# Optimization experiments

Hardware: AMD Instinct MI355X
Metric: run time of the kernel (lower is better)

The kernel has to match this reference:

```python
import jax, jax.numpy as jnp
import numpy as np

D_MODEL = 1024
N_HEADS = 16
D_K = D_MODEL // N_HEADS
EPS = 1e-8


def _l2_rownorm(x):
    # RowNormActivation: normalize each row (last dim) to unit L2 norm
    return x * jax.lax.rsqrt(jnp.sum(x * x, axis=-1, keepdims=True) + EPS)


def setup_inputs() -> dict:
    key = jax.random.key(0)
    ks = jax.random.split(key, 11)
    B, S = 2, 2048
    sc = 1.0 / np.sqrt(D_MODEL)
    inp = {
        "Q": jax.random.normal(ks[0], (B, S, D_MODEL), jnp.float32),
        "K": jax.random.normal(ks[1], (B, S, D_MODEL), jnp.float32),
        "V": jax.random.normal(ks[2], (B, S, D_MODEL), jnp.float32),
        "Wq_w": jax.random.normal(ks[3], (D_MODEL, D_MODEL), jnp.float32) * sc,
        "Wq_b": jnp.zeros((D_MODEL,), jnp.float32),
        "Wk_w": jax.random.normal(ks[4], (D_MODEL, D_MODEL), jnp.float32) * sc,
        "Wk_b": jnp.zeros((D_MODEL,), jnp.float32),
        "Wv_w": jax.random.normal(ks[5], (D_MODEL, D_MODEL), jnp.float32) * sc,
        "Wv_b": jnp.zeros((D_MODEL,), jnp.float32),
        "Wo_w": jax.random.normal(ks[6], (D_MODEL, D_MODEL), jnp.float32) * sc,
        "Wo_b": jnp.zeros((D_MODEL,), jnp.float32),
    }
    return inp


def reference(Q, K, V, Wq_w, Wq_b, Wk_w, Wk_b, Wv_w, Wv_b, Wo_w, Wo_b):
    B, S, _ = Q.shape
    # torch Linear: y = x @ W.T + b
    q = (Q @ Wq_w.T + Wq_b).reshape(B, S, N_HEADS, D_K).transpose(0, 2, 1, 3)
    k = (K @ Wk_w.T + Wk_b).reshape(B, S, N_HEADS, D_K).transpose(0, 2, 1, 3)
    v = (V @ Wv_w.T + Wv_b).reshape(B, S, N_HEADS, D_K).transpose(0, 2, 1, 3)
    qn = _l2_rownorm(q)
    kn = _l2_rownorm(k)
    scores = jnp.einsum("bhqd,bhkd->bhqk", qn, kn)
    attn = scores * scores  # squared similarity, no softmax (dropout=0 / eval)
    out = jnp.einsum("bhqk,bhkd->bhqd", attn, v)
    out = out.transpose(0, 2, 1, 3).reshape(B, S, D_MODEL)
    return out @ Wo_w.T + Wo_b
```

## Files before the change

kernel.cpp:

```cpp
#include <hip/hip_runtime.h>
#include <hip/hip_bf16.h>


#define D_MODEL 1024
#define N_HEADS 16
#define D_K     64
#define BATCH   2
#define SEQ     2048
#define M_TOT   (BATCH * SEQ)

typedef short  s16x8 __attribute__((ext_vector_type(8)));
typedef float  f32x4 __attribute__((ext_vector_type(4)));
typedef unsigned short ushort_t;
typedef ushort_t us4 __attribute__((ext_vector_type(4)));

__device__ __forceinline__ ushort_t f2bf(float f) {
    union { float f; unsigned int u; } x; x.f = f;
    unsigned int u = x.u;
    return (ushort_t)((u + 0x7fffu + ((u >> 16) & 1u)) >> 16);
}
__device__ __forceinline__ float bf2f(ushort_t h) {
    union { unsigned int u; float f; } x; x.u = ((unsigned int)h) << 16;
    return x.f;
}
__device__ __forceinline__ unsigned int pack2bf(float a, float b) {
    union { __hip_bfloat162 h; unsigned int u; } x;
    x.h = __float22bfloat162_rn(float2{a, b});
    return x.u;
}

__device__ __forceinline__ void gload_lds16(const ushort_t* g, ushort_t* l) {
    __builtin_amdgcn_global_load_lds(
        (__attribute__((address_space(1))) void*)(ushort_t*)g,
        (__attribute__((address_space(3))) void*)l, 16, 0, 0);
}

#define WAIT_VM(n)  asm volatile("s_waitcnt vmcnt(" #n ")" ::: "memory")
#define WAIT_LGKM0  asm volatile("s_waitcnt lgkmcnt(0)" ::: "memory")
#define BARRIER     asm volatile("s_barrier" ::: "memory")

struct ConvArgs {
    const float* src[11];
    ushort_t*    dst[11];
    int          n[11];
};

__global__ __launch_bounds__(256) void convert_kernel(ConvArgs a) {
    const int t = blockIdx.y;
    const int i = (blockIdx.x * 256 + threadIdx.x) * 4;
    if (i >= a.n[t]) return;
    const float4 v = *(const float4*)(a.src[t] + i);
    us4 p;
    p[0] = f2bf(v.x); p[1] = f2bf(v.y); p[2] = f2bf(v.z); p[3] = f2bf(v.w);
    *(us4*)(a.dst[t] + i) = p;
}

template <int BM, int MODE>
__device__ __forceinline__ void gemm_body(
    ushort_t* __restrict__ smem,
    const ushort_t* __restrict__ A,
    const ushort_t* __restrict__ W,
    const ushort_t* __restrict__ bias,
    ushort_t* __restrict__ out,
    float* __restrict__ outf,
    int bx, int by)
{
    static_assert(BM == 64 || BM == 128, "");
    constexpr int K    = 1024;
    constexpr int MF   = BM / 32;
    constexpr int BUFW = (BM + 128) * 64;
    constexpr int NIT  = K / 64;

    const int t    = threadIdx.x;
    const int wave = t >> 6;
    const int lane = t & 63;
    const int quad = lane >> 4;
    const int lc   = lane & 15;
    const int wm   = wave >> 1;
    const int wn   = wave & 1;
    const int m0   = bx * BM;
    const int n0   = by * 128;

    f32x4 acc[MF][4];
    const f32x4 zero = {0.f, 0.f, 0.f, 0.f};
#pragma unroll
    for (int i = 0; i < MF; ++i)
#pragma unroll
        for (int j = 0; j < 4; ++j) acc[i][j] = zero;

    auto stage = [&](int buf, int k0) {
        ushort_t* Ast = smem + buf * BUFW;
        ushort_t* Bst = Ast + BM * 64;
#pragma unroll
        for (int c = 0; c < MF; ++c) {
            int idx = c * 256 + t;
            int row = idx >> 3, phys = idx & 7;
            int col = (phys ^ (row & 7)) * 8;
            gload_lds16(A + (size_t)(m0 + row) * K + k0 + col, Ast + idx * 8);
        }
#pragma unroll
        for (int c = 0; c < 4; ++c) {
            int idx = c * 256 + t;
            int row = idx >> 3, phys = idx & 7;
            int col = (phys ^ (row & 7)) * 8;
            gload_lds16(W + (size_t)(n0 + row) * K + k0 + col, Bst + idx * 8);
        }
    };
    auto comp = [&](int buf) {
        ushort_t* Ast = smem + buf * BUFW;
        ushort_t* Bst = Ast + BM * 64;
#pragma unroll
        for (int ks = 0; ks < 2; ++ks) {
            const int ph = ((ks * 4 + quad) ^ (lc & 7)) * 8;
            s16x8 a[MF], b[4];
#pragma unroll
            for (int i = 0; i < MF; ++i)
                a[i] = *(const s16x8*)(Ast + (wm * (BM / 2) + i * 16 + lc) * 64 + ph);
#pragma unroll
            for (int i = 0; i < 4; ++i)
                b[i] = *(const s16x8*)(Bst + (wn * 64 + i * 16 + lc) * 64 + ph);
#pragma unroll
            for (int mf = 0; mf < MF; ++mf)
#pragma unroll
                for (int nf = 0; nf < 4; ++nf)
                    acc[mf][nf] = __builtin_amdgcn_mfma_f32_16x16x32_bf16(
                        a[mf], b[nf], acc[mf][nf], 0, 0, 0);
        }
    };

    stage(0, 0);
    stage(1, 64);
    for (int it = 0; it < NIT - 2; ++it) {
        if constexpr (BM == 128) WAIT_VM(8); else WAIT_VM(6);
        BARRIER;
        comp(it & 1);
        WAIT_LGKM0;
        BARRIER;
        stage(it & 1, (it + 2) * 64);
    }
    if constexpr (BM == 128) WAIT_VM(8); else WAIT_VM(6);
    BARRIER;
    comp((NIT - 2) & 1);
    WAIT_VM(0);
    BARRIER;
    comp((NIT - 1) & 1);

    float bv[4];
#pragma unroll
    for (int nf = 0; nf < 4; ++nf) bv[nf] = bf2f(bias[n0 + wn * 64 + nf * 16 + lc]);

    if (MODE == 0) {
#pragma unroll
        for (int mf = 0; mf < MF; ++mf)
#pragma unroll
            for (int nf = 0; nf < 4; ++nf)
#pragma unroll
                for (int r = 0; r < 4; ++r) {
                    int mg = m0 + wm * (BM / 2) + mf * 16 + quad * 4 + r;
                    int ng = n0 + wn * 64 + nf * 16 + lc;
                    outf[(size_t)mg * D_MODEL + ng] = acc[mf][nf][r] + bv[nf];
                }
    } else if (MODE == 1) {
#pragma unroll
        for (int mf = 0; mf < MF; ++mf)
#pragma unroll
            for (int r = 0; r < 4; ++r) {
                float ss = 0.f;
#pragma unroll
                for (int nf = 0; nf < 4; ++nf) {
                    float v = acc[mf][nf][r] + bv[nf];
                    acc[mf][nf][r] = v;
                    ss += v * v;
                }
                ss += __shfl_xor(ss, 1);
                ss += __shfl_xor(ss, 2);
                ss += __shfl_xor(ss, 4);
                ss += __shfl_xor(ss, 8);
                float inv = rsqrtf(ss + 1e-8f);
                int mg = m0 + wm * (BM / 2) + mf * 16 + quad * 4 + r;
                int b  = mg >> 11;
                int s  = mg & 2047;
#pragma unroll
                for (int nf = 0; nf < 4; ++nf) {
                    int ng = n0 + wn * 64 + nf * 16 + lc;
                    int h = ng >> 6, d = ng & 63;
                    out[(((size_t)(b * N_HEADS + h)) * SEQ + s) * D_K + d] =
                        f2bf(acc[mf][nf][r] * inv);
                }
            }
    } else {
        __syncthreads();
        ushort_t* vt = smem + wave * (64 * 72);
#pragma unroll
        for (int mf = 0; mf < 4; ++mf)
#pragma unroll
            for (int nf = 0; nf < 4; ++nf) {
                us4 p;
#pragma unroll
                for (int r = 0; r < 4; ++r) p[r] = f2bf(acc[mf][nf][r] + bv[nf]);
                *(us4*)(vt + (nf * 16 + lc) * 72 + mf * 16 + quad * 4) = p;
            }
        WAIT_LGKM0;
#pragma unroll
        for (int r = 0; r < 8; ++r) {
            int d  = r * 8 + (lane >> 3);
            int so = (lane & 7) * 8;
            uint4 val = *(const uint4*)(vt + d * 72 + so);
            int mg = m0 + wm * 64 + so;
            int b  = mg >> 11;
            int s  = mg & 2047;
            int ng = n0 + wn * 64 + d;
            int h = ng >> 6, dh = ng & 63;
            *(uint4*)(out + (((size_t)(b * N_HEADS + h)) * D_K + dh) * SEQ + s) = val;
        }
    }
}

__global__ __launch_bounds__(256) void qkv_kernel(
    const ushort_t* __restrict__ Qb, const ushort_t* __restrict__ Kb,
    const ushort_t* __restrict__ Vb,
    const ushort_t* __restrict__ Wq, const ushort_t* __restrict__ Wk,
    const ushort_t* __restrict__ Wv,
    const ushort_t* __restrict__ bq, const ushort_t* __restrict__ bk,
    const ushort_t* __restrict__ bv,
    ushort_t* __restrict__ qn, ushort_t* __restrict__ kn,
    ushort_t* __restrict__ vT)
{
    __shared__ __align__(16) ushort_t smem[2 * (128 + 128) * 64];
    const int z = blockIdx.z;
    if (z == 0)
        gemm_body<128, 1>(smem, Qb, Wq, bq, qn, nullptr, blockIdx.x, blockIdx.y);
    else if (z == 1)
        gemm_body<128, 1>(smem, Kb, Wk, bk, kn, nullptr, blockIdx.x, blockIdx.y);
    else
        gemm_body<128, 2>(smem, Vb, Wv, bv, vT, nullptr, blockIdx.x, blockIdx.y);
}

__global__ __launch_bounds__(256) void wo_kernel(
    const ushort_t* __restrict__ A, const ushort_t* __restrict__ W,
    const ushort_t* __restrict__ bias, float* __restrict__ outf)
{
    __shared__ __align__(16) ushort_t smem[2 * (64 + 128) * 64];
    gemm_body<64, 0>(smem, A, W, bias, nullptr, outf, blockIdx.x, blockIdx.y);
}

__global__ __launch_bounds__(256) void attn_kernel(
    const ushort_t* __restrict__ qn,
    const ushort_t* __restrict__ kn,
    const ushort_t* __restrict__ vT,
    ushort_t* __restrict__ attn_out)
{
    __shared__ __align__(16) ushort_t smem[2 * 8192];
    __shared__ __align__(16) ushort_t Pl[128 * 64];

    const int t    = threadIdx.x;
    const int wave = t >> 6;
    const int lane = t & 63;
    const int quad = lane >> 4;
    const int lc   = lane & 15;
    const int bh   = blockIdx.x;
    const int qt   = blockIdx.y;
    const int b    = bh >> 4;
    const int h    = bh & 15;

    const ushort_t* qb = qn + (size_t)bh * SEQ * D_K;
    const ushort_t* kb = kn + (size_t)bh * SEQ * D_K;
    const ushort_t* vb = vT + (size_t)bh * D_K * SEQ;
    const int q0 = qt * 128;

    s16x8 qf[8][2];
#pragma unroll
    for (int mf = 0; mf < 8; ++mf)
#pragma unroll
        for (int ks = 0; ks < 2; ++ks)
            qf[mf][ks] = *(const s16x8*)(qb + (size_t)(q0 + mf * 16 + lc) * D_K +
                                         ks * 32 + quad * 8);

    f32x4 oacc[2][4];
    const f32x4 zero = {0.f, 0.f, 0.f, 0.f};
#pragma unroll
    for (int mf = 0; mf < 2; ++mf)
#pragma unroll
        for (int df = 0; df < 4; ++df) oacc[mf][df] = zero;

    auto stage = [&](int buf, int j0) {
        ushort_t* kst = smem + buf * 8192;
        ushort_t* vst = kst + 4096;
#pragma unroll
        for (int c = 0; c < 2; ++c) {
            int idx = c * 256 + t;
            int row = idx >> 3, phys = idx & 7;
            int col = (phys ^ (row & 7)) * 8;
            gload_lds16(kb + (size_t)(j0 + row) * D_K + col, kst + idx * 8);
            gload_lds16(vb + (size_t)row * SEQ + j0 + col, vst + idx * 8);
        }
    };

    auto qk = [&](int buf) {
        ushort_t* kst = smem + buf * 8192;
        s16x8 ak[2];
#pragma unroll
        for (int ks = 0; ks < 2; ++ks)
            ak[ks] = *(const s16x8*)(kst + (wave * 16 + lc) * 64 +
                                     (((ks * 4 + quad) ^ (lc & 7)) * 8));
        const int log8 = wave * 4 + quad;
#pragma unroll
        for (int mf = 0; mf < 8; ++mf) {
            f32x4 st = zero;
#pragma unroll
            for (int ks = 0; ks < 2; ++ks)
                st = __builtin_amdgcn_mfma_f32_16x16x32_bf16(ak[ks], qf[mf][ks], st, 0, 0, 0);
            uint2 w;
            w.x = pack2bf(st[0] * st[0], st[1] * st[1]);
            w.y = pack2bf(st[2] * st[2], st[3] * st[3]);
            const int row = mf * 16 + lc;
            *(uint2*)(Pl + row * 64 + (log8 ^ lc) * 4) = w;
        }
    };

    auto pv = [&](int buf) {
        ushort_t* vst = smem + buf * 8192 + 4096;
        s16x8 bvf[4][2];
#pragma unroll
        for (int df = 0; df < 4; ++df)
#pragma unroll
            for (int ks = 0; ks < 2; ++ks)
                bvf[df][ks] = *(const s16x8*)(vst + (df * 16 + lc) * 64 +
                                              (((ks * 4 + quad) ^ (lc & 7)) * 8));
        s16x8 aa[2][2];
#pragma unroll
        for (int mfp = 0; mfp < 2; ++mfp)
#pragma unroll
            for (int ks = 0; ks < 2; ++ks) {
                const int row = wave * 32 + mfp * 16 + lc;
                const int l0  = ks * 8 + quad * 2;
                uint2 lo = *(const uint2*)(Pl + row * 64 + ((l0 ^ lc) * 4));
                uint2 hi = *(const uint2*)(Pl + row * 64 + (((l0 + 1) ^ lc) * 4));
                union { unsigned int u[4]; s16x8 v; } m;
                m.u[0] = lo.x; m.u[1] = lo.y; m.u[2] = hi.x; m.u[3] = hi.y;
                aa[mfp][ks] = m.v;
            }
#pragma unroll
        for (int mfp = 0; mfp < 2; ++mfp)
#pragma unroll
            for (int df = 0; df < 4; ++df)
#pragma unroll
                for (int ks = 0; ks < 2; ++ks)
                    oacc[mfp][df] = __builtin_amdgcn_mfma_f32_16x16x32_bf16(
                        aa[mfp][ks], bvf[df][ks], oacc[mfp][df], 0, 0, 0);
    };

    constexpr int NT = 32;
    stage(0, 0);
    stage(1, 64);
    for (int it = 0; it < NT; ++it) {
        if (it < NT - 1) { WAIT_VM(4); } else { WAIT_VM(0); }
        BARRIER;
        qk(it & 1);
        WAIT_LGKM0;
        BARRIER;
        pv(it & 1);
        if (it < NT - 2) {
            WAIT_LGKM0;
            BARRIER;
            stage(it & 1, (it + 2) * 64);
        } else if (it == NT - 2) {
            WAIT_LGKM0;
            BARRIER;
        }
    }

#pragma unroll
    for (int mfp = 0; mfp < 2; ++mfp)
#pragma unroll
        for (int df = 0; df < 4; ++df)
#pragma unroll
            for (int r = 0; r < 4; ++r) {
                int s = q0 + wave * 32 + mfp * 16 + quad * 4 + r;
                int d = df * 16 + lc;
                attn_out[((size_t)(b * SEQ + s)) * D_MODEL + h * D_K + d] =
                    f2bf(oacc[mfp][df][r]);
            }
}

extern "C" void kernel_launch(void* const* d_in, const int* in_sizes, int n_in,
                              void* d_out, int out_size, void* d_ws, size_t ws_size,
                              hipStream_t stream)
{
    const float* Qf   = (const float*)d_in[0];
    const float* Kf   = (const float*)d_in[1];
    const float* Vf   = (const float*)d_in[2];
    const float* Wqf  = (const float*)d_in[3];
    const float* Wqbf = (const float*)d_in[4];
    const float* Wkf  = (const float*)d_in[5];
    const float* Wkbf = (const float*)d_in[6];
    const float* Wvf  = (const float*)d_in[7];
    const float* Wvbf = (const float*)d_in[8];
    const float* Wof  = (const float*)d_in[9];
    const float* Wobf = (const float*)d_in[10];

    const size_t NM = (size_t)M_TOT * D_MODEL;
    const size_t NW = (size_t)D_MODEL * D_MODEL;
    const size_t NB = D_MODEL;

    ushort_t* p = (ushort_t*)d_ws;
    ushort_t* Qb  = p;  p += NM;
    ushort_t* Kb  = p;  p += NM;
    ushort_t* Vb  = p;  p += NM;
    ushort_t* Wq  = p;  p += NW;
    ushort_t* Wk  = p;  p += NW;
    ushort_t* Wv  = p;  p += NW;
    ushort_t* Wo  = p;  p += NW;
    ushort_t* bq  = p;  p += NB;
    ushort_t* bk  = p;  p += NB;
    ushort_t* bvv = p;  p += NB;
    ushort_t* bo  = p;  p += NB;
    ushort_t* qn  = p;  p += NM;
    ushort_t* kn  = p;  p += NM;
    ushort_t* vT  = p;  p += NM;
    ushort_t* ao  = p;  p += NM;

    ConvArgs ca;
    ca.src[0] = Qf;   ca.dst[0] = Qb;  ca.n[0] = (int)NM;
    ca.src[1] = Kf;   ca.dst[1] = Kb;  ca.n[1] = (int)NM;
    ca.src[2] = Vf;   ca.dst[2] = Vb;  ca.n[2] = (int)NM;
    ca.src[3] = Wqf;  ca.dst[3] = Wq;  ca.n[3] = (int)NW;
    ca.src[4] = Wkf;  ca.dst[4] = Wk;  ca.n[4] = (int)NW;
    ca.src[5] = Wvf;  ca.dst[5] = Wv;  ca.n[5] = (int)NW;
    ca.src[6] = Wof;  ca.dst[6] = Wo;  ca.n[6] = (int)NW;
    ca.src[7] = Wqbf; ca.dst[7] = bq;  ca.n[7] = (int)NB;
    ca.src[8] = Wkbf; ca.dst[8] = bk;  ca.n[8] = (int)NB;
    ca.src[9] = Wvbf; ca.dst[9] = bvv; ca.n[9] = (int)NB;
    ca.src[10] = Wobf; ca.dst[10] = bo; ca.n[10] = (int)NB;

    dim3 blk(256);
    convert_kernel<<<dim3((unsigned)(NM / (256 * 4)), 11), blk, 0, stream>>>(ca);

    qkv_kernel<<<dim3(M_TOT / 128, D_MODEL / 128, 3), blk, 0, stream>>>(
        Qb, Kb, Vb, Wq, Wk, Wv, bq, bk, bvv, qn, kn, vT);
    attn_kernel<<<dim3(BATCH * N_HEADS, SEQ / 128), blk, 0, stream>>>(qn, kn, vT, ao);
    wo_kernel<<<dim3(M_TOT / 64, D_MODEL / 128), blk, 0, stream>>>(
        ao, Wo, bo, (float*)d_out);
}
```

Measured before the change: 224.4 us.

## Keep attention probabilities in registers and split KV across waves with reduction

The attention kernel no longer writes the squared scores to shared memory for the PV product. Each wave now computes P for its own 16-key slice and feeds it straight into 16x16x16 MFMAs, accumulating partial outputs for all 128 queries, which are then reduced across the four waves through shared memory at the end. The K/V staging grows from a double buffer to a four-deep buffer with fewer barriers per iteration, and launch bounds request two blocks per SIMD. In exchange it uses many more accumulator registers (32 f32x4 per lane), MFMAs with half the K depth, and an extra cross-wave reduction epilogue.

```diff
diff --git a/kernel.cpp b/kernel.cpp
--- a/kernel.cpp
+++ b/kernel.cpp
@@ -10,6 +10,7 @@
 #define M_TOT   (BATCH * SEQ)
 
 typedef short  s16x8 __attribute__((ext_vector_type(8)));
+typedef short  s16x4 __attribute__((ext_vector_type(4)));
 typedef float  f32x4 __attribute__((ext_vector_type(4)));
 typedef unsigned short ushort_t;
 typedef ushort_t us4 __attribute__((ext_vector_type(4)));
@@ -27,6 +28,16 @@
     union { __hip_bfloat162 h; unsigned int u; } x;
     x.h = __float22bfloat162_rn(float2{a, b});
     return x.u;
+}
+
+__device__ __forceinline__ f32x4 mfma_pv(s16x4 a, s16x4 b, f32x4 c) {
+#if __has_builtin(__builtin_amdgcn_mfma_f32_16x16x16bf16_1k)
+    return __builtin_amdgcn_mfma_f32_16x16x16bf16_1k(a, b, c, 0, 0, 0);
+#else
+    s16x8 a8 = {a[0], a[1], a[2], a[3], 0, 0, 0, 0};
+    s16x8 b8 = {b[0], b[1], b[2], b[3], 0, 0, 0, 0};
+    return __builtin_amdgcn_mfma_f32_16x16x32_bf16(a8, b8, c, 0, 0, 0);
+#endif
 }
 
 __device__ __forceinline__ void gload_lds16(const ushort_t* g, ushort_t* l) {
@@ -244,14 +255,13 @@
     gemm_body<64, 0>(smem, A, W, bias, nullptr, outf, blockIdx.x, blockIdx.y);
 }
 
-__global__ __launch_bounds__(256) void attn_kernel(
+__global__ __launch_bounds__(256, 2) void attn_kernel(
     const ushort_t* __restrict__ qn,
     const ushort_t* __restrict__ kn,
     const ushort_t* __restrict__ vT,
     ushort_t* __restrict__ attn_out)
 {
-    __shared__ __align__(16) ushort_t smem[2 * 8192];
-    __shared__ __align__(16) ushort_t Pl[128 * 64];
+    __shared__ __align__(16) ushort_t smem[4 * 8192];
 
     const int t    = threadIdx.x;
     const int wave = t >> 6;
@@ -276,12 +286,12 @@
             qf[mf][ks] = *(const s16x8*)(qb + (size_t)(q0 + mf * 16 + lc) * D_K +
                                          ks * 32 + quad * 8);
 
-    f32x4 oacc[2][4];
+    f32x4 oacc[4][8];
     const f32x4 zero = {0.f, 0.f, 0.f, 0.f};
 #pragma unroll
-    for (int mf = 0; mf < 2; ++mf)
-#pragma unroll
-        for (int df = 0; df < 4; ++df) oacc[mf][df] = zero;
+    for (int df = 0; df < 4; ++df)
+#pragma unroll
+        for (int mf = 0; mf < 8; ++mf) oacc[df][mf] = zero;
 
     auto stage = [&](int buf, int j0) {
         ushort_t* kst = smem + buf * 8192;
@@ -296,91 +306,74 @@
         }
     };
 
-    auto qk = [&](int buf) {
+    auto compute = [&](int buf) {
         ushort_t* kst = smem + buf * 8192;
+        ushort_t* vst = kst + 4096;
         s16x8 ak[2];
 #pragma unroll
         for (int ks = 0; ks < 2; ++ks)
             ak[ks] = *(const s16x8*)(kst + (wave * 16 + lc) * 64 +
                                      (((ks * 4 + quad) ^ (lc & 7)) * 8));
-        const int log8 = wave * 4 + quad;
+        s16x4 av[4];
+#pragma unroll
+        for (int df = 0; df < 4; ++df) {
+            const int d  = df * 16 + lc;
+            const int cj = wave * 2 + (quad >> 1);
+            av[df] = *(const s16x4*)(vst + d * 64 + ((cj ^ (d & 7)) << 3) +
+                                     ((quad & 1) << 2));
+        }
 #pragma unroll
         for (int mf = 0; mf < 8; ++mf) {
             f32x4 st = zero;
 #pragma unroll
             for (int ks = 0; ks < 2; ++ks)
-                st = __builtin_amdgcn_mfma_f32_16x16x32_bf16(ak[ks], qf[mf][ks], st, 0, 0, 0);
-            uint2 w;
-            w.x = pack2bf(st[0] * st[0], st[1] * st[1]);
-            w.y = pack2bf(st[2] * st[2], st[3] * st[3]);
-            const int row = mf * 16 + lc;
-            *(uint2*)(Pl + row * 64 + (log8 ^ lc) * 4) = w;
-        }
-    };
-
-    auto pv = [&](int buf) {
-        ushort_t* vst = smem + buf * 8192 + 4096;
-        s16x8 bvf[4][2];
-#pragma unroll
-        for (int df = 0; df < 4; ++df)
-#pragma unroll
-            for (int ks = 0; ks < 2; ++ks)
-                bvf[df][ks] = *(const s16x8*)(vst + (df * 16 + lc) * 64 +
-                                              (((ks * 4 + quad) ^ (lc & 7)) * 8));
-        s16x8 aa[2][2];
-#pragma unroll
-        for (int mfp = 0; mfp < 2; ++mfp)
-#pragma unroll
-            for (int ks = 0; ks < 2; ++ks) {
-                const int row = wave * 32 + mfp * 16 + lc;
-                const int l0  = ks * 8 + quad * 2;
-                uint2 lo = *(const uint2*)(Pl + row * 64 + ((l0 ^ lc) * 4));
-                uint2 hi = *(const uint2*)(Pl + row * 64 + (((l0 + 1) ^ lc) * 4));
-                union { unsigned int u[4]; s16x8 v; } m;
-                m.u[0] = lo.x; m.u[1] = lo.y; m.u[2] = hi.x; m.u[3] = hi.y;
-                aa[mfp][ks] = m.v;
-            }
-#pragma unroll
-        for (int mfp = 0; mfp < 2; ++mfp)
+                st = __builtin_amdgcn_mfma_f32_16x16x32_bf16(ak[ks], qf[mf][ks],
+                                                             st, 0, 0, 0);
+            union { unsigned int u[2]; s16x4 v; } pb;
+            pb.u[0] = pack2bf(st[0] * st[0], st[1] * st[1]);
+            pb.u[1] = pack2bf(st[2] * st[2], st[3] * st[3]);
 #pragma unroll
             for (int df = 0; df < 4; ++df)
-#pragma unroll
-                for (int ks = 0; ks < 2; ++ks)
-                    oacc[mfp][df] = __builtin_amdgcn_mfma_f32_16x16x32_bf16(
-                        aa[mfp][ks], bvf[df][ks], oacc[mfp][df], 0, 0, 0);
+                oacc[df][mf] = mfma_pv(av[df], pb.v, oacc[df][mf]);
+        }
     };
 
     constexpr int NT = 32;
     stage(0, 0);
     stage(1, 64);
+    stage(2, 128);
     for (int it = 0; it < NT; ++it) {
-        if (it < NT - 1) { WAIT_VM(4); } else { WAIT_VM(0); }
+        if (it < NT - 2)      { WAIT_VM(8); }
+        else if (it == NT - 2){ WAIT_VM(4); }
+        else                  { WAIT_VM(0); }
         BARRIER;
-        qk(it & 1);
+        compute(it & 3);
+        if (it < NT - 3) stage((it + 3) & 3, (it + 3) * 64);
+    }
+
+    float* red = (float*)smem;
+    constexpr int RP = 17;
+#pragma unroll
+    for (int mf = 0; mf < 8; ++mf) {
+        BARRIER;
+#pragma unroll
+        for (int df = 0; df < 4; ++df)
+#pragma unroll
+            for (int r = 0; r < 4; ++r)
+                red[(wave * 64 + df * 16 + quad * 4 + r) * RP + lc] =
+                    oacc[df][mf][r];
         WAIT_LGKM0;
         BARRIER;
-        pv(it & 1);
-        if (it < NT - 2) {
-            WAIT_LGKM0;
-            BARRIER;
-            stage(it & 1, (it + 2) * 64);
-        } else if (it == NT - 2) {
-            WAIT_LGKM0;
-            BARRIER;
+#pragma unroll
+        for (int qq = 0; qq < 4; ++qq) {
+            const int q = wave * 4 + qq;
+            const int d = lane;
+            float v = red[(0 * 64 + d) * RP + q] + red[(1 * 64 + d) * RP + q] +
+                      red[(2 * 64 + d) * RP + q] + red[(3 * 64 + d) * RP + q];
+            const int s = q0 + mf * 16 + q;
+            attn_out[((size_t)(b * SEQ + s)) * D_MODEL + h * D_K + d] = f2bf(v);
         }
     }
-
-#pragma unroll
-    for (int mfp = 0; mfp < 2; ++mfp)
-#pragma unroll
-        for (int df = 0; df < 4; ++df)
-#pragma unroll
-            for (int r = 0; r < 4; ++r) {
-                int s = q0 + wave * 32 + mfp * 16 + quad * 4 + r;
-                int d = df * 16 + lc;
-                attn_out[((size_t)(b * SEQ + s)) * D_MODEL + h * D_K + d] =
-                    f2bf(oacc[mfp][df][r]);
-            }
 }
 
 extern "C" void kernel_launch(void* const* d_in, const int* in_sizes, int n_in,
```

Measured after the change: 220.7 us. About the same (-1.6%).
